# Kernel tuning notes

Hardware: AMD Instinct MI355X
Metric: run time of the kernel (lower is better)

The kernel has to match this reference:

```python
import jax, jax.numpy as jnp
import numpy as np

EPS_KERNEL = 1e-4   # eps added inside softmax_kernel exp
EPS_DENOM = 1e-6    # eps added to k_cumsum in the denominator
N_CHUNKS = 128      # matches torch.chunk(128, dim=-2) in causal_linear_attention_noncuda


def gaussian_orthogonal_random_matrix(nb_rows, nb_cols, rng):
    # scaling=0: rows are orthogonal blocks scaled by chi-distributed norms
    n_full = nb_rows // nb_cols + (1 if nb_rows % nb_cols else 0)
    blocks = []
    for _ in range(n_full):
        g = rng.standard_normal((nb_cols, nb_cols))
        qmat, _ = np.linalg.qr(g)
        blocks.append(qmat.T)
    mat = np.concatenate(blocks, axis=0)[:nb_rows]
    multiplier = np.linalg.norm(rng.standard_normal((nb_rows, nb_cols)), axis=1)
    return (multiplier[:, None] * mat).astype(np.float32)


def softmax_kernel(x, proj, is_query):
    # x: [b,h,n,d], proj: [m,d] -> phi(x): [b,h,n,m]
    d = x.shape[-1]
    normalizer = d ** -0.25
    ratio = proj.shape[0] ** -0.5
    xd = jnp.einsum('bhnd,md->bhnm', normalizer * x, proj)
    diag = 0.5 * (normalizer ** 2) * jnp.sum(x * x, axis=-1, keepdims=True)  # [b,h,n,1]
    if is_query:
        mx = jnp.max(xd, axis=-1, keepdims=True)
    else:
        mx = jnp.max(xd, axis=(-1, -2), keepdims=True)
    return ratio * (jnp.exp(xd - diag - mx) + EPS_KERNEL)


def causal_linear_attention(q, k, v):
    # q,k: [b,h,n,m] phi-features; v: [b,h,n,d]
    b, h, n, m = q.shape
    d = v.shape[-1]
    c = n // N_CHUNKS  # chunk length

    def chunked(t):
        return jnp.moveaxis(t.reshape(b, h, N_CHUNKS, c, t.shape[-1]), 2, 0)

    qc, kc, vc = chunked(q), chunked(k), chunked(v)  # [nc,b,h,c,*]

    def step(carry, inp):
        k_last, ctx_last = carry  # [b,h,m], [b,h,m,d]
        qi, ki, vi = inp
        k_cum = k_last[:, :, None, :] + jnp.cumsum(ki, axis=2)            # [b,h,c,m]
        d_inv = 1.0 / jnp.einsum('bhcm,bhcm->bhc', qi, k_cum + EPS_DENOM)
        ctx = jnp.einsum('bhcm,bhcd->bhcmd', ki, vi)                      # [b,h,c,m,d]
        ctx_cum = ctx_last[:, :, None, :, :] + jnp.cumsum(ctx, axis=2)
        out = jnp.einsum('bhcmd,bhcm,bhc->bhcd', ctx_cum, qi, d_inv)
        return (k_cum[:, :, -1], ctx_cum[:, :, -1]), out

    init = (jnp.zeros((b, h, m), q.dtype), jnp.zeros((b, h, m, d), q.dtype))
    _, outs = jax.lax.scan(jax.checkpoint(step), init, (qc, kc, vc))
    return jnp.moveaxis(outs, 0, 2).reshape(b, h, n, d)


def setup_inputs() -> dict:
    key = jax.random.key(0)
    kq, kk, kv = jax.random.split(key, 3)
    shape = (2, 8, 2048, 64)  # [batch, heads, seq, dim_heads]
    q = jax.random.normal(kq, shape, dtype=jnp.float32)
    k = jax.random.normal(kk, shape, dtype=jnp.float32)
    v = jax.random.normal(kv, shape, dtype=jnp.float32)
    proj = jnp.asarray(gaussian_orthogonal_random_matrix(256, 64, np.random.default_rng(0)))
    return {"q": q, "k": k, "v": v, "projection_matrix": proj}


def reference(q, k, v, projection_matrix):
    q_prime = softmax_kernel(q, projection_matrix, is_query=True)
    k_prime = softmax_kernel(k, projection_matrix, is_query=False)
    return causal_linear_attention(q_prime, k_prime, v)
```

## Files before the change

kernel.cpp:

```cpp
#include <hip/hip_runtime.h>
#include <hip/hip_bf16.h>
#include <cstddef>

typedef __attribute__((ext_vector_type(8))) short bf16x8;
typedef __attribute__((ext_vector_type(4))) float f32x4;

#define NCH_ 512
#define NRM_ 0.35355339059327373f
#define RATIO_ 0.0625f
#define EPSC_ 6.25e-6f
#define MFMA(a,b,c) __builtin_amdgcn_mfma_f32_16x16x32_bf16((a),(b),(c),0,0,0)

__device__ __forceinline__ unsigned short f2b(float f) {
  unsigned u = __float_as_uint(f);
  u += 0x7FFFu + ((u >> 16) & 1u);
  return (unsigned short)(u >> 16);
}
__device__ __forceinline__ float b2f(unsigned short h) {
  return __uint_as_float(((unsigned)h) << 16);
}
__device__ __forceinline__ unsigned pk2f(float a, float b) {
  union { __hip_bfloat162 h; unsigned u; } cv;
  cv.h = __float22bfloat162_rn(make_float2(a, b));
  return cv.u;
}
__device__ __forceinline__ float sumsq4(float4 a){ return a.x*a.x+a.y*a.y+a.z*a.z+a.w*a.w; }

__device__ __forceinline__ void arrive(unsigned* cnt) {
  __syncthreads();
  if (threadIdx.x == 0) {
    __threadfence();
    __hip_atomic_fetch_add(cnt, 1u, __ATOMIC_RELEASE, __HIP_MEMORY_SCOPE_AGENT);
  }
}
__device__ __forceinline__ void wait_for(unsigned* cnt, unsigned goal) {
  if (threadIdx.x == 0) {
    while (__hip_atomic_load(cnt, __ATOMIC_RELAXED, __HIP_MEMORY_SCOPE_AGENT) < goal)
      __builtin_amdgcn_s_sleep(4);
    __threadfence();
  }
  __syncthreads();
}

__global__ __launch_bounds__(256, 2) void fused_kernel(
    const float* __restrict__ qg, const float* __restrict__ kg,
    const float* __restrict__ vg, const float* __restrict__ projg,
    unsigned short* __restrict__ kvxP, unsigned short* __restrict__ sxP,
    float* __restrict__ blockmax, float* __restrict__ vsumG,
    float* __restrict__ out_g, unsigned* __restrict__ cnts)
{
  __shared__ unsigned short R0[256*72];
  __shared__ unsigned short XB[128*72];
  __shared__ unsigned short C_[80*72];
  __shared__ float diagK[64];
  __shared__ float diagQ[64];
  __shared__ float rmS[4*64];
  __shared__ float cmS[4];
  __shared__ float schS;
  const int t=threadIdx.x, ch=blockIdx.x;
  const int row0 = ch*64;
  const int lane=t&63, m16=lane&15, q4=lane>>4, w=t>>6;
  const int f0 = w*64, r0 = w*16;
  const int bh_own = ch>>5;
  unsigned* cntA = cnts;
  unsigned* cntS = cnts + 16;
  unsigned short* KX = XB;
  unsigned short* QX = XB + 64*72;
  unsigned short* kpT = XB;

#pragma unroll
  for (int i=0;i<8;++i){ int flat=i*2048+t*8; int f=flat>>6, d2=flat&63;
    float4 p0 = *(const float4*)(projg+flat);
    float4 p1 = *(const float4*)(projg+flat+4);
    *(uint4*)&R0[f*72+d2] = make_uint4(pk2f(p0.x,p0.y),pk2f(p0.z,p0.w),
                                       pk2f(p1.x,p1.y),pk2f(p1.z,p1.w)); }
  {
    const float* xg = kg + (size_t)row0*64;
#pragma unroll
    for (int i=0;i<4;++i){
      int flat=i*1024+t*4; int r=flat>>6, d2=flat&63;
      float4 f = *(const float4*)(xg+flat);
      float ss = sumsq4(f);
      ss += __shfl_xor(ss,1); ss += __shfl_xor(ss,2);
      ss += __shfl_xor(ss,4); ss += __shfl_xor(ss,8);
      if ((t&15)==0) diagK[r] = 0.0625f*ss;
      *(uint2*)&KX[r*72+d2] = make_uint2(pk2f(NRM_*f.x,NRM_*f.y), pk2f(NRM_*f.z,NRM_*f.w));
    }
  }
  {
    const float* xg = qg + (size_t)row0*64;
#pragma unroll
    for (int i=0;i<4;++i){
      int flat=i*1024+t*4; int r=flat>>6, d2=flat&63;
      float4 f = *(const float4*)(xg+flat);
      float ss = sumsq4(f);
      ss += __shfl_xor(ss,1); ss += __shfl_xor(ss,2);
      ss += __shfl_xor(ss,4); ss += __shfl_xor(ss,8);
      if ((t&15)==0) diagQ[r] = 0.0625f*ss;
      *(uint2*)&QX[r*72+d2] = make_uint2(pk2f(NRM_*f.x,NRM_*f.y), pk2f(NRM_*f.z,NRM_*f.w));
    }
  }
  {
    int c = t&63, sq_ = t>>6;
#pragma unroll
    for (int i=0;i<16;++i)
      C_[c*72 + sq_*16 + i] = f2b(vg[((size_t)row0 + sq_*16 + i)*64 + c]);
    int cc = 64 + (t>>4), s4 = (t&15)*4;
    unsigned short hv = (cc==64) ? (unsigned short)0x3F80 : (unsigned short)0;
    unsigned pv = (unsigned)hv | ((unsigned)hv<<16);
    *(uint2*)&C_[cc*72 + s4] = make_uint2(pv, pv);
  }
  __syncthreads();

  if (t < 80) {
    float s = 0.f;
#pragma unroll 16
    for (int i=0;i<64;++i) s += b2f(C_[t*72+i]);
    vsumG[(size_t)ch*80 + t] = s;
  }

  bf16x8 bk[4][2], bq[4][2]; float dk4[4], dq4[4];
#pragma unroll
  for (int rt=0;rt<4;++rt){
    bk[rt][0] = *(const bf16x8*)&KX[(rt*16+m16)*72 + q4*8];
    bk[rt][1] = *(const bf16x8*)&KX[(rt*16+m16)*72 + 32 + q4*8];
    bq[rt][0] = *(const bf16x8*)&QX[(rt*16+m16)*72 + q4*8];
    bq[rt][1] = *(const bf16x8*)&QX[(rt*16+m16)*72 + 32 + q4*8];
    dk4[rt] = diagK[rt*16+m16];
    dq4[rt] = diagQ[rt*16+m16];
  }
  f32x4 kacc[4][4], qacc[4][4];
#pragma unroll
  for (int rt=0;rt<4;++rt)
#pragma unroll
    for (int mt=0;mt<4;++mt){ kacc[rt][mt] = (f32x4){0.f,0.f,0.f,0.f};
                              qacc[rt][mt] = (f32x4){0.f,0.f,0.f,0.f}; }
#pragma unroll
  for (int kk=0;kk<2;++kk)
#pragma unroll
    for (int mt=0;mt<4;++mt){
      bf16x8 a = *(const bf16x8*)&R0[(f0+mt*16+m16)*72 + kk*32 + q4*8];
#pragma unroll
      for (int rt=0;rt<4;++rt){
        kacc[rt][mt] = MFMA(a, bk[rt][kk], kacc[rt][mt]);
        qacc[rt][mt] = MFMA(a, bq[rt][kk], qacc[rt][mt]);
      }
    }
  {
    float mx = kacc[0][0][0];
#pragma unroll
    for (int rt=0;rt<4;++rt)
#pragma unroll
      for (int mt=0;mt<4;++mt)
#pragma unroll
        for (int j=0;j<4;++j) mx = fmaxf(mx, kacc[rt][mt][j]);
#pragma unroll
    for (int off=1; off<64; off<<=1) mx = fmaxf(mx, __shfl_xor(mx, off));
    if (lane == 0) cmS[w] = mx;
  }
#pragma unroll
  for (int rt=0;rt<4;++rt){
    float p = qacc[rt][0][0];
#pragma unroll
    for (int mt=0;mt<4;++mt)
#pragma unroll
      for (int j=0;j<4;++j) p = fmaxf(p, qacc[rt][mt][j]);
    p = fmaxf(p, __shfl_xor(p,16)); p = fmaxf(p, __shfl_xor(p,32));
    if (q4 == 0) rmS[w*64 + rt*16+m16] = p;
  }
  __syncthreads();
  const float cmax = fmaxf(fmaxf(cmS[0],cmS[1]),fmaxf(cmS[2],cmS[3]));
  if (t == 0) blockmax[ch] = cmax;

  unsigned short* qS = R0;
#pragma unroll
  for (int rt=0;rt<4;++rt){
    int rr = rt*16+m16;
    float rm = fmaxf(fmaxf(rmS[rr],rmS[64+rr]),fmaxf(rmS[128+rr],rmS[192+rr]));
    float e = dq4[rt] + rm;
#pragma unroll
    for (int mt=0;mt<4;++mt){
      float v0 = RATIO_*(__expf(qacc[rt][mt][0]-e)+1e-4f);
      float v1 = RATIO_*(__expf(qacc[rt][mt][1]-e)+1e-4f);
      float v2 = RATIO_*(__expf(qacc[rt][mt][2]-e)+1e-4f);
      float v3 = RATIO_*(__expf(qacc[rt][mt][3]-e)+1e-4f);
      *(uint2*)&qS[rr*264 + f0 + mt*16 + q4*4] = make_uint2(pk2f(v0,v1), pk2f(v2,v3));
    }
  }
  __syncthreads();
  bf16x8 aq[8];
#pragma unroll
  for (int kk=0;kk<8;++kk)
    aq[kk] = *(const bf16x8*)&qS[(r0+m16)*264 + kk*32 + q4*8];
  float q1v = 0.f;
#pragma unroll
  for (int kk=0;kk<8;++kk){
    union { bf16x8 v; unsigned u[4]; } av; av.v = aq[kk];
#pragma unroll
    for (int i=0;i<4;++i)
      q1v += b2f((unsigned short)av.u[i]) + b2f((unsigned short)(av.u[i]>>16));
  }
  q1v += __shfl_xor(q1v,16); q1v += __shfl_xor(q1v,32);
  __syncthreads();

  unsigned short* kpS = R0;
  unsigned kpx[4][4][2];
#pragma unroll
  for (int rt=0;rt<4;++rt){
    float e = dk4[rt] + cmax;
    int rr = rt*16+m16;
#pragma unroll
    for (int mt=0;mt<4;++mt){
      float v0 = RATIO_*__expf(kacc[rt][mt][0]-e);
      float v1 = RATIO_*__expf(kacc[rt][mt][1]-e);
      float v2 = RATIO_*__expf(kacc[rt][mt][2]-e);
      float v3 = RATIO_*__expf(kacc[rt][mt][3]-e);
      kpx[rt][mt][0] = pk2f(v0,v1); kpx[rt][mt][1] = pk2f(v2,v3);
      *(uint2*)&kpS[rr*264 + f0 + mt*16 + q4*4] = make_uint2(kpx[rt][mt][0], kpx[rt][mt][1]);
    }
  }
  if ((w>>1) == 0) {
#pragma unroll
    for (int rt=0;rt<4;++rt)
#pragma unroll
      for (int mt=0;mt<4;++mt)
#pragma unroll
        for (int jp=0;jp<2;++jp){
          int frl = (w&1)*64 + mt*16 + q4*4 + jp*2;
          unsigned uv = kpx[rt][mt][jp];
          kpT[frl*72 + rt*16+m16]     = (unsigned short)uv;
          kpT[(frl+1)*72 + rt*16+m16] = (unsigned short)(uv>>16);
        }
  }
  __syncthreads();
#pragma unroll
  for (int h=0; h<2; ++h) {
    if (h == 1) {
      __syncthreads();
      if ((w>>1) == 1) {
#pragma unroll
        for (int rt=0;rt<4;++rt)
#pragma unroll
          for (int mt=0;mt<4;++mt)
#pragma unroll
            for (int jp=0;jp<2;++jp){
              int frl = (w&1)*64 + mt*16 + q4*4 + jp*2;
              unsigned uv = kpx[rt][mt][jp];
              kpT[frl*72 + rt*16+m16]     = (unsigned short)uv;
              kpT[(frl+1)*72 + rt*16+m16] = (unsigned short)(uv>>16);
            }
      }
      __syncthreads();
    }
    f32x4 c2a[5][2];
#pragma unroll
    for (int ct=0;ct<5;++ct)
#pragma unroll
      for (int p=0;p<2;++p) c2a[ct][p] = (f32x4){0.f,0.f,0.f,0.f};
#pragma unroll
    for (int kk=0;kk<2;++kk){
      bf16x8 av[5];
#pragma unroll
      for (int ct=0;ct<5;++ct)
        av[ct] = *(const bf16x8*)&C_[(ct*16+m16)*72 + kk*32 + q4*8];
#pragma unroll
      for (int p=0;p<2;++p){
        int mtl = w*2 + p;
        bf16x8 bv = *(const bf16x8*)&kpT[(mtl*16+m16)*72 + kk*32 + q4*8];
#pragma unroll
        for (int ct=0;ct<5;++ct)
          c2a[ct][p] = MFMA(av[ct], bv, c2a[ct][p]);
      }
    }
#pragma unroll
    for (int ct=0;ct<5;++ct)
#pragma unroll
      for (int p=0;p<2;++p){
        int mtg = h*8 + w*2 + p;
        int mrow = mtg*16 + m16;
        int fb = (mrow>>5)*512 + ((mrow>>3)&3)*8 + (mrow&7);
        unsigned short* dst = kvxP + (size_t)(ch*5+ct)*4096 + fb + (q4*4)*32;
#pragma unroll
        for (int j=0;j<4;++j)
          dst[j*32] = f2b(c2a[ct][p][j]);
      }
    if (h == 0) __syncthreads();
  }

  arrive(&cntA[bh_own]);

  if (ch < 320) {
    const int qtr = ch & 3, ct5 = (ch>>2)%5, bhs = ch/20;
    wait_for(&cntA[bhs], 32u);
    float* sS  = (float*)XB;
    float* vsS = ((float*)XB) + 32;
    if (t < 32) {
      float bm = blockmax[bhs*32 + t];
      float km = bm;
#pragma unroll
      for (int off=16; off>=1; off>>=1) km = fmaxf(km, __shfl_xor(km, off));
      sS[t] = __expf(bm - km);
    }
    for (int i=t; i<512; i+=256){
      int chl = i>>4, c16 = i&15;
      vsS[chl*16+c16] = vsumG[(size_t)(bhs*32+chl)*80 + ct5*16 + c16];
    }
    __syncthreads();
    const int fbase = qtr*1024 + t*4;
    const int c16t = (t>>3)&15;
    const bool isEps = (ct5==4) && (c16t == 1);
    float carry0=0.f, carry1=0.f, carry2=0.f, carry3=0.f;
    const size_t stride = (size_t)5*4096;
    size_t base = ((size_t)(bhs*32)*5 + ct5)*4096 + fbase;
#pragma unroll 8
    for (int chl=0; chl<32; ++chl){
      unsigned s0, s1;
      if (isEps) { unsigned ee = pk2f(1e-6f,1e-6f); s0 = ee; s1 = ee; }
      else { s0 = pk2f(carry0,carry1); s1 = pk2f(carry2,carry3); }
      *(uint2*)(sxP + base) = make_uint2(s0, s1);
      uint2 raw = *(const uint2*)(kvxP + base);
      float sc_ = sS[chl];
      float evs = EPSC_ * vsS[chl*16+c16t];
      carry0 += sc_*b2f((unsigned short)(raw.x))     + evs;
      carry1 += sc_*b2f((unsigned short)(raw.x>>16)) + evs;
      carry2 += sc_*b2f((unsigned short)(raw.y))     + evs;
      carry3 += sc_*b2f((unsigned short)(raw.y>>16)) + evs;
      base += stride;
    }
    arrive(&cntS[bhs]);
  }

  wait_for(&cntS[bh_own], 20u);

  if (t < 32) {
    float bm = blockmax[bh_own*32 + t];
    float km = bm;
#pragma unroll
    for (int off=16; off>=1; off>>=1) km = fmaxf(km, __shfl_xor(km, off));
    if (t == (ch & 31)) schS = __expf(bm - km);
  }

  f32x4 accA[4], accO[5];
#pragma unroll
  for (int i=0;i<4;++i) accA[i] = (f32x4){0.f,0.f,0.f,0.f};
#pragma unroll
  for (int i=0;i<5;++i) accO[i] = (f32x4){0.f,0.f,0.f,0.f};
  const unsigned short* sxb = sxP + (size_t)ch*5*4096 + m16*32 + q4*8;
#pragma unroll
  for (int kk=0;kk<8;++kk){
    bf16x8 a = aq[kk];
#pragma unroll
    for (int st=0;st<4;++st){
      bf16x8 bfr = *(const bf16x8*)&kpS[(st*16+m16)*264 + kk*32 + q4*8];
      accA[st] = MFMA(a, bfr, accA[st]);
    }
#pragma unroll
    for (int ct=0;ct<5;++ct)
      accO[ct] = MFMA(a, *(const bf16x8*)(sxb + (size_t)ct*4096 + kk*512), accO[ct]);
  }
  __syncthreads();
  const float sch = schS;
  unsigned short* P = XB;
#pragma unroll
  for (int j=0;j<4;++j){
    int rr = r0 + q4*4 + j;
    float q1r = __shfl(q1v, q4*4 + j);
    float addc = EPSC_ * q1r;
#pragma unroll
    for (int st=0;st<4;++st){
      int cc = st*16 + m16;
      P[rr*72 + cc] = f2b((cc<=rr) ? (sch*accA[st][j] + addc) : 0.f);
    }
  }
#pragma unroll
  for (int k2=0;k2<2;++k2){
    bf16x8 aP = *(const bf16x8*)&P[(r0+m16)*72 + k2*32 + q4*8];
#pragma unroll
    for (int ct=0;ct<5;++ct){
      bf16x8 bfr = *(const bf16x8*)&C_[(ct*16+m16)*72 + k2*32 + q4*8];
      accO[ct] = MFMA(aP, bfr, accO[ct]);
    }
  }
  __syncthreads();
  float* oT = (float*)R0;
#pragma unroll
  for (int j=0;j<4;++j){
    float d64 = __shfl(accO[4][j], (lane & 48));
    float d65 = __shfl(accO[4][j], (lane & 48) | 1);
    float dinv = 1.f/(d64+d65);
    int rr = r0 + q4*4 + j;
#pragma unroll
    for (int ct=0;ct<4;++ct)
      oT[rr*68 + ct*16 + m16] = accO[ct][j]*dinv;
  }
  __syncthreads();
#pragma unroll
  for (int i=0;i<4;++i){ int flat=i*1024+t*4; int r=flat>>6, c2=flat&63;
    *(float4*)(out_g + (size_t)row0*64 + flat) = *(const float4*)&oT[r*68+c2]; }
}


__global__ __launch_bounds__(256, 2) void kfeat_kernel(
    const float* __restrict__ kg, const float* __restrict__ vg,
    const float* __restrict__ projg,
    unsigned short* __restrict__ kvxP,
    float* __restrict__ blockmax, float* __restrict__ vsumG)
{
  __shared__ unsigned short R0[256*72];
  __shared__ unsigned short XB[128*72];
  __shared__ unsigned short C_[80*72];
  __shared__ float diagS[64];
  __shared__ float rmS[4];
  const int t=threadIdx.x, ch=blockIdx.x;
  const int row0 = ch*64;
  const int lane=t&63, m16=lane&15, q4=lane>>4, w=t>>6;
  const int f0 = w*64;
  unsigned short* kpS = R0;
  unsigned short* xbS = XB;
  unsigned short* kpT = XB;

#pragma unroll
  for (int i=0;i<8;++i){ int flat=i*2048+t*8; int f=flat>>6, d2=flat&63;
    float4 p0 = *(const float4*)(projg+flat);
    float4 p1 = *(const float4*)(projg+flat+4);
    *(uint4*)&R0[f*72+d2] = make_uint4(pk2f(p0.x,p0.y),pk2f(p0.z,p0.w),
                                       pk2f(p1.x,p1.y),pk2f(p1.z,p1.w)); }
  {
    const float* xg = kg + (size_t)row0*64;
#pragma unroll
    for (int i=0;i<4;++i){
      int flat=i*1024+t*4; int r=flat>>6, d2=flat&63;
      float4 f = *(const float4*)(xg+flat);
      float ss = sumsq4(f);
      ss += __shfl_xor(ss,1); ss += __shfl_xor(ss,2);
      ss += __shfl_xor(ss,4); ss += __shfl_xor(ss,8);
      if ((t&15)==0) diagS[r] = 0.0625f*ss;
      *(uint2*)&xbS[r*72+d2] = make_uint2(pk2f(NRM_*f.x,NRM_*f.y), pk2f(NRM_*f.z,NRM_*f.w));
    }
  }
  {
    int c = t&63, sq_ = t>>6;
#pragma unroll
    for (int i=0;i<16;++i)
      C_[c*72 + sq_*16 + i] = f2b(vg[((size_t)row0 + sq_*16 + i)*64 + c]);
    int cc = 64 + (t>>4), s4 = (t&15)*4;
    unsigned short hv = (cc==64) ? (unsigned short)0x3F80 : (unsigned short)0;
    unsigned pv = (unsigned)hv | ((unsigned)hv<<16);
    *(uint2*)&C_[cc*72 + s4] = make_uint2(pv, pv);
  }
  __syncthreads();

  if (t < 80) {
    float s = 0.f;
#pragma unroll 16
    for (int i=0;i<64;++i) s += b2f(C_[t*72+i]);
    vsumG[(size_t)ch*80 + t] = s;
  }

  bf16x8 b[4][2]; float diag4[4];
#pragma unroll
  for (int rt=0;rt<4;++rt){
    b[rt][0] = *(const bf16x8*)&xbS[(rt*16+m16)*72 + q4*8];
    b[rt][1] = *(const bf16x8*)&xbS[(rt*16+m16)*72 + 32 + q4*8];
    diag4[rt] = diagS[rt*16+m16];
  }
  f32x4 acc[4][4];
#pragma unroll
  for (int rt=0;rt<4;++rt)
#pragma unroll
    for (int mt=0;mt<4;++mt) acc[rt][mt] = (f32x4){0.f,0.f,0.f,0.f};
#pragma unroll
  for (int kk=0;kk<2;++kk)
#pragma unroll
    for (int mt=0;mt<4;++mt){
      bf16x8 a = *(const bf16x8*)&R0[(f0+mt*16+m16)*72 + kk*32 + q4*8];
#pragma unroll
      for (int rt=0;rt<4;++rt)
        acc[rt][mt] = MFMA(a, b[rt][kk], acc[rt][mt]);
    }
  {
    float mx = acc[0][0][0];
#pragma unroll
    for (int rt=0;rt<4;++rt)
#pragma unroll
      for (int mt=0;mt<4;++mt)
#pragma unroll
        for (int j=0;j<4;++j) mx = fmaxf(mx, acc[rt][mt][j]);
#pragma unroll
    for (int off=1; off<64; off<<=1) mx = fmaxf(mx, __shfl_xor(mx, off));
    if (lane == 0) rmS[w] = mx;
  }
  __syncthreads();
  const float cmax = fmaxf(fmaxf(rmS[0],rmS[1]),fmaxf(rmS[2],rmS[3]));
  if (t == 0) blockmax[ch] = cmax;

  unsigned kpx[4][4][2];
#pragma unroll
  for (int rt=0;rt<4;++rt){
    float e = diag4[rt] + cmax;
    int rr = rt*16+m16;
#pragma unroll
    for (int mt=0;mt<4;++mt){
      float v0 = RATIO_*__expf(acc[rt][mt][0]-e);
      float v1 = RATIO_*__expf(acc[rt][mt][1]-e);
      float v2 = RATIO_*__expf(acc[rt][mt][2]-e);
      float v3 = RATIO_*__expf(acc[rt][mt][3]-e);
      kpx[rt][mt][0] = pk2f(v0,v1); kpx[rt][mt][1] = pk2f(v2,v3);
      *(uint2*)&kpS[rr*264 + f0 + mt*16 + q4*4] = make_uint2(kpx[rt][mt][0], kpx[rt][mt][1]);
    }
  }
  if ((w>>1) == 0) {
#pragma unroll
    for (int rt=0;rt<4;++rt)
#pragma unroll
      for (int mt=0;mt<4;++mt)
#pragma unroll
        for (int jp=0;jp<2;++jp){
          int frl = (w&1)*64 + mt*16 + q4*4 + jp*2;
          unsigned uv = kpx[rt][mt][jp];
          kpT[frl*72 + rt*16+m16]     = (unsigned short)uv;
          kpT[(frl+1)*72 + rt*16+m16] = (unsigned short)(uv>>16);
        }
  }
  __syncthreads();
#pragma unroll
  for (int h=0; h<2; ++h) {
    if (h == 1) {
      __syncthreads();
      if ((w>>1) == 1) {
#pragma unroll
        for (int rt=0;rt<4;++rt)
#pragma unroll
          for (int mt=0;mt<4;++mt)
#pragma unroll
            for (int jp=0;jp<2;++jp){
              int frl = (w&1)*64 + mt*16 + q4*4 + jp*2;
              unsigned uv = kpx[rt][mt][jp];
              kpT[frl*72 + rt*16+m16]     = (unsigned short)uv;
              kpT[(frl+1)*72 + rt*16+m16] = (unsigned short)(uv>>16);
            }
      }
      __syncthreads();
    }
    f32x4 c2a[5][2];
#pragma unroll
    for (int ct=0;ct<5;++ct)
#pragma unroll
      for (int p=0;p<2;++p) c2a[ct][p] = (f32x4){0.f,0.f,0.f,0.f};
#pragma unroll
    for (int kk=0;kk<2;++kk){
      bf16x8 av[5];
#pragma unroll
      for (int ct=0;ct<5;++ct)
        av[ct] = *(const bf16x8*)&C_[(ct*16+m16)*72 + kk*32 + q4*8];
#pragma unroll
      for (int p=0;p<2;++p){
        int mtl = w*2 + p;
        bf16x8 bv = *(const bf16x8*)&kpT[(mtl*16+m16)*72 + kk*32 + q4*8];
#pragma unroll
        for (int ct=0;ct<5;++ct)
          c2a[ct][p] = MFMA(av[ct], bv, c2a[ct][p]);
      }
    }
#pragma unroll
    for (int ct=0;ct<5;++ct)
#pragma unroll
      for (int p=0;p<2;++p){
        int mtg = h*8 + w*2 + p;
        int mrow = mtg*16 + m16;
        int fb = (mrow>>5)*512 + ((mrow>>3)&3)*8 + (mrow&7);
        unsigned short* dst = kvxP + (size_t)(ch*5+ct)*4096 + fb + (q4*4)*32;
#pragma unroll
        for (int j=0;j<4;++j)
          dst[j*32] = f2b(c2a[ct][p][j]);
      }
    if (h == 0) __syncthreads();
  }
}

__global__ __launch_bounds__(256, 4) void scan_kernel(
    const unsigned short* __restrict__ kvxP, unsigned short* __restrict__ sxP,
    const float* __restrict__ blockmax, const float* __restrict__ vsumG)
{
  __shared__ float sS[32];
  __shared__ float vsS[32][16];
  const int t = threadIdx.x, bid = blockIdx.x;
  const int qtr = bid & 3, ct = (bid>>2)%5, bh = bid/20;
  if (t < 32) {
    float bm = blockmax[bh*32 + t];
    float km = bm;
#pragma unroll
    for (int off=16; off>=1; off>>=1) km = fmaxf(km, __shfl_xor(km, off));
    sS[t] = __expf(bm - km);
  }
  for (int i=t; i<512; i+=256){
    int chl = i>>4, c16 = i&15;
    vsS[chl][c16] = vsumG[(size_t)(bh*32+chl)*80 + ct*16 + c16];
  }
  __syncthreads();
  const int fbase = qtr*1024 + t*4;
  const int c16t = (t>>3)&15;
  const bool isEps = (ct==4) && (c16t == 1);
  float carry0=0.f, carry1=0.f, carry2=0.f, carry3=0.f;
  const size_t stride = (size_t)5*4096;
  size_t base = ((size_t)(bh*32)*5 + ct)*4096 + fbase;
#pragma unroll 4
  for (int chl=0; chl<32; ++chl){
    unsigned s0, s1;
    if (isEps) { unsigned ee = pk2f(1e-6f,1e-6f); s0 = ee; s1 = ee; }
    else { s0 = pk2f(carry0,carry1); s1 = pk2f(carry2,carry3); }
    *(uint2*)(sxP + base) = make_uint2(s0, s1);
    uint2 raw = *(const uint2*)(kvxP + base);
    float sch = sS[chl];
    float evs = EPSC_ * vsS[chl][c16t];
    carry0 += sch*b2f((unsigned short)(raw.x))     + evs;
    carry1 += sch*b2f((unsigned short)(raw.x>>16)) + evs;
    carry2 += sch*b2f((unsigned short)(raw.y))     + evs;
    carry3 += sch*b2f((unsigned short)(raw.y>>16)) + evs;
    base += stride;
  }
}

__global__ __launch_bounds__(256, 2) void out_kernel(
    const float* __restrict__ qg, const float* __restrict__ kg,
    const float* __restrict__ projg, const unsigned short* __restrict__ sxP,
    const float* __restrict__ vg, const float* __restrict__ blockmax,
    float* __restrict__ out_g)
{
  __shared__ unsigned short R0[256*72];
  __shared__ unsigned short KX[64*72];
  __shared__ unsigned short QX[64*72];
  __shared__ unsigned short C_[80*72];
  __shared__ float diagK[64];
  __shared__ float diagQ[64];
  __shared__ float rmS[4*64];
  __shared__ float cmS[4];
  __shared__ float schS;
  const int t=threadIdx.x, ch=blockIdx.x;
  const int row0 = ch*64;
  const int lane=t&63, m16=lane&15, q4=lane>>4, w=t>>6;
  const int f0 = w*64, r0 = w*16;
  unsigned short* P = KX;

#pragma unroll
  for (int i=0;i<8;++i){ int flat=i*2048+t*8; int f=flat>>6, d2=flat&63;
    float4 p0 = *(const float4*)(projg+flat);
    float4 p1 = *(const float4*)(projg+flat+4);
    *(uint4*)&R0[f*72+d2] = make_uint4(pk2f(p0.x,p0.y),pk2f(p0.z,p0.w),
                                       pk2f(p1.x,p1.y),pk2f(p1.z,p1.w)); }
  {
    const float* xg = kg + (size_t)row0*64;
#pragma unroll
    for (int i=0;i<4;++i){
      int flat=i*1024+t*4; int r=flat>>6, d2=flat&63;
      float4 f = *(const float4*)(xg+flat);
      float ss = sumsq4(f);
      ss += __shfl_xor(ss,1); ss += __shfl_xor(ss,2);
      ss += __shfl_xor(ss,4); ss += __shfl_xor(ss,8);
      if ((t&15)==0) diagK[r] = 0.0625f*ss;
      *(uint2*)&KX[r*72+d2] = make_uint2(pk2f(NRM_*f.x,NRM_*f.y), pk2f(NRM_*f.z,NRM_*f.w));
    }
  }
  {
    const float* xg = qg + (size_t)row0*64;
#pragma unroll
    for (int i=0;i<4;++i){
      int flat=i*1024+t*4; int r=flat>>6, d2=flat&63;
      float4 f = *(const float4*)(xg+flat);
      float ss = sumsq4(f);
      ss += __shfl_xor(ss,1); ss += __shfl_xor(ss,2);
      ss += __shfl_xor(ss,4); ss += __shfl_xor(ss,8);
      if ((t&15)==0) diagQ[r] = 0.0625f*ss;
      *(uint2*)&QX[r*72+d2] = make_uint2(pk2f(NRM_*f.x,NRM_*f.y), pk2f(NRM_*f.z,NRM_*f.w));
    }
  }
  {
    int c = t&63, sq_ = t>>6;
#pragma unroll
    for (int i=0;i<16;++i)
      C_[c*72 + sq_*16 + i] = f2b(vg[((size_t)row0 + sq_*16 + i)*64 + c]);
    int cc = 64 + (t>>4), s4 = (t&15)*4;
    unsigned short hv = (cc==64) ? (unsigned short)0x3F80 : (unsigned short)0;
    unsigned pv = (unsigned)hv | ((unsigned)hv<<16);
    *(uint2*)&C_[cc*72 + s4] = make_uint2(pv, pv);
  }
  if (t < 32) {
    float bm = blockmax[(ch>>5)*32 + t];
    float km = bm;
#pragma unroll
    for (int off=16; off>=1; off>>=1) km = fmaxf(km, __shfl_xor(km, off));
    if (t == (ch & 31)) schS = __expf(bm - km);
  }
  __syncthreads();

  bf16x8 bk[4][2], bq[4][2]; float dk4[4], dq4[4];
#pragma unroll
  for (int rt=0;rt<4;++rt){
    bk[rt][0] = *(const bf16x8*)&KX[(rt*16+m16)*72 + q4*8];
    bk[rt][1] = *(const bf16x8*)&KX[(rt*16+m16)*72 + 32 + q4*8];
    bq[rt][0] = *(const bf16x8*)&QX[(rt*16+m16)*72 + q4*8];
    bq[rt][1] = *(const bf16x8*)&QX[(rt*16+m16)*72 + 32 + q4*8];
    dk4[rt] = diagK[rt*16+m16];
    dq4[rt] = diagQ[rt*16+m16];
  }
  f32x4 kacc[4][4], qacc[4][4];
#pragma unroll
  for (int rt=0;rt<4;++rt)
#pragma unroll
    for (int mt=0;mt<4;++mt){ kacc[rt][mt] = (f32x4){0.f,0.f,0.f,0.f};
                              qacc[rt][mt] = (f32x4){0.f,0.f,0.f,0.f}; }
#pragma unroll
  for (int kk=0;kk<2;++kk)
#pragma unroll
    for (int mt=0;mt<4;++mt){
      bf16x8 a = *(const bf16x8*)&R0[(f0+mt*16+m16)*72 + kk*32 + q4*8];
#pragma unroll
      for (int rt=0;rt<4;++rt){
        kacc[rt][mt] = MFMA(a, bk[rt][kk], kacc[rt][mt]);
        qacc[rt][mt] = MFMA(a, bq[rt][kk], qacc[rt][mt]);
      }
    }
  {
    float mx = kacc[0][0][0];
#pragma unroll
    for (int rt=0;rt<4;++rt)
#pragma unroll
      for (int mt=0;mt<4;++mt)
#pragma unroll
        for (int j=0;j<4;++j) mx = fmaxf(mx, kacc[rt][mt][j]);
#pragma unroll
    for (int off=1; off<64; off<<=1) mx = fmaxf(mx, __shfl_xor(mx, off));
    if (lane == 0) cmS[w] = mx;
  }
#pragma unroll
  for (int rt=0;rt<4;++rt){
    float p = qacc[rt][0][0];
#pragma unroll
    for (int mt=0;mt<4;++mt)
#pragma unroll
      for (int j=0;j<4;++j) p = fmaxf(p, qacc[rt][mt][j]);
    p = fmaxf(p, __shfl_xor(p,16)); p = fmaxf(p, __shfl_xor(p,32));
    if (q4 == 0) rmS[w*64 + rt*16+m16] = p;
  }
  __syncthreads();
  const float cmax = fmaxf(fmaxf(cmS[0],cmS[1]),fmaxf(cmS[2],cmS[3]));

  unsigned short* qS = R0;
#pragma unroll
  for (int rt=0;rt<4;++rt){
    int rr = rt*16+m16;
    float rm = fmaxf(fmaxf(rmS[rr],rmS[64+rr]),fmaxf(rmS[128+rr],rmS[192+rr]));
    float e = dq4[rt] + rm;
#pragma unroll
    for (int mt=0;mt<4;++mt){
      float v0 = RATIO_*(__expf(qacc[rt][mt][0]-e)+1e-4f);
      float v1 = RATIO_*(__expf(qacc[rt][mt][1]-e)+1e-4f);
      float v2 = RATIO_*(__expf(qacc[rt][mt][2]-e)+1e-4f);
      float v3 = RATIO_*(__expf(qacc[rt][mt][3]-e)+1e-4f);
      *(uint2*)&qS[rr*264 + f0 + mt*16 + q4*4] = make_uint2(pk2f(v0,v1), pk2f(v2,v3));
    }
  }
  __syncthreads();
  bf16x8 aq[8];
#pragma unroll
  for (int kk=0;kk<8;++kk)
    aq[kk] = *(const bf16x8*)&qS[(r0+m16)*264 + kk*32 + q4*8];
  float q1v = 0.f;
#pragma unroll
  for (int kk=0;kk<8;++kk){
    union { bf16x8 v; unsigned u[4]; } av; av.v = aq[kk];
#pragma unroll
    for (int i=0;i<4;++i)
      q1v += b2f((unsigned short)av.u[i]) + b2f((unsigned short)(av.u[i]>>16));
  }
  q1v += __shfl_xor(q1v,16); q1v += __shfl_xor(q1v,32);
  __syncthreads();

  unsigned short* kpS = R0;
#pragma unroll
  for (int rt=0;rt<4;++rt){
    float e = dk4[rt] + cmax;
    int rr = rt*16+m16;
#pragma unroll
    for (int mt=0;mt<4;++mt){
      float v0 = RATIO_*__expf(kacc[rt][mt][0]-e);
      float v1 = RATIO_*__expf(kacc[rt][mt][1]-e);
      float v2 = RATIO_*__expf(kacc[rt][mt][2]-e);
      float v3 = RATIO_*__expf(kacc[rt][mt][3]-e);
      *(uint2*)&kpS[rr*264 + f0 + mt*16 + q4*4] = make_uint2(pk2f(v0,v1), pk2f(v2,v3));
    }
  }
  __syncthreads();

  f32x4 accA[4], accO[5];
#pragma unroll
  for (int i=0;i<4;++i) accA[i] = (f32x4){0.f,0.f,0.f,0.f};
#pragma unroll
  for (int i=0;i<5;++i) accO[i] = (f32x4){0.f,0.f,0.f,0.f};
  const unsigned short* sxb = sxP + (size_t)ch*5*4096 + m16*32 + q4*8;
#pragma unroll
  for (int kk=0;kk<8;++kk){
    bf16x8 a = aq[kk];
#pragma unroll
    for (int st=0;st<4;++st){
      bf16x8 bfr = *(const bf16x8*)&kpS[(st*16+m16)*264 + kk*32 + q4*8];
      accA[st] = MFMA(a, bfr, accA[st]);
    }
#pragma unroll
    for (int ct=0;ct<5;++ct)
      accO[ct] = MFMA(a, *(const bf16x8*)(sxb + (size_t)ct*4096 + kk*512), accO[ct]);
  }
  __syncthreads();
  const float sch = schS;
#pragma unroll
  for (int j=0;j<4;++j){
    int rr = r0 + q4*4 + j;
    float q1r = __shfl(q1v, q4*4 + j);
    float addc = EPSC_ * q1r;
#pragma unroll
    for (int st=0;st<4;++st){
      int cc = st*16 + m16;
      P[rr*72 + cc] = f2b((cc<=rr) ? (sch*accA[st][j] + addc) : 0.f);
    }
  }
#pragma unroll
  for (int k2=0;k2<2;++k2){
    bf16x8 aP = *(const bf16x8*)&P[(r0+m16)*72 + k2*32 + q4*8];
#pragma unroll
    for (int ct=0;ct<5;++ct){
      bf16x8 bfr = *(const bf16x8*)&C_[(ct*16+m16)*72 + k2*32 + q4*8];
      accO[ct] = MFMA(aP, bfr, accO[ct]);
    }
  }
  __syncthreads();
  float* oT = (float*)R0;
#pragma unroll
  for (int j=0;j<4;++j){
    float d64 = __shfl(accO[4][j], (lane & 48));
    float d65 = __shfl(accO[4][j], (lane & 48) | 1);
    float dinv = 1.f/(d64+d65);
    int rr = r0 + q4*4 + j;
#pragma unroll
    for (int ct=0;ct<4;++ct)
      oT[rr*68 + ct*16 + m16] = accO[ct][j]*dinv;
  }
  __syncthreads();
#pragma unroll
  for (int i=0;i<4;++i){ int flat=i*1024+t*4; int r=flat>>6, c2=flat&63;
    *(float4*)(out_g + (size_t)row0*64 + flat) = *(const float4*)&oT[r*68+c2]; }
}

extern "C" void kernel_launch(void* const* d_in, const int* in_sizes, int n_in,
                              void* d_out, int out_size, void* d_ws, size_t ws_size,
                              hipStream_t stream)
{
  (void)in_sizes; (void)n_in; (void)out_size; (void)ws_size;
  const float* q    = (const float*)d_in[0];
  const float* k    = (const float*)d_in[1];
  const float* v    = (const float*)d_in[2];
  const float* proj = (const float*)d_in[3];
  float* out = (float*)d_out;

  char* p8 = (char*)d_ws;
  unsigned short* kvxP = (unsigned short*)p8; p8 += (size_t)NCH_*5*4096*2;
  unsigned short* sxP  = (unsigned short*)p8; p8 += (size_t)NCH_*5*4096*2;
  float* blockmax = (float*)p8; p8 += NCH_*sizeof(float);
  float* vsumG    = (float*)p8; p8 += (size_t)NCH_*80*sizeof(float);
  unsigned* cnts  = (unsigned*)p8;

  static int fused_ok = -1;
  if (fused_ok < 0) {
    int nb = 0;
    hipError_t e = hipOccupancyMaxActiveBlocksPerMultiprocessor(&nb, fused_kernel,
                                                                256, (size_t)0);
    fused_ok = (e == hipSuccess && nb >= 2) ? 1 : 0;
  }

  if (fused_ok) {
    hipMemsetAsync(cnts, 0, 32*sizeof(unsigned), stream);
    fused_kernel<<<dim3(NCH_), dim3(256), 0, stream>>>(q, k, v, proj, kvxP, sxP,
                                                       blockmax, vsumG, out, cnts);
  } else {
    kfeat_kernel<<<dim3(NCH_), dim3(256), 0, stream>>>(k, v, proj, kvxP,
                                                       blockmax, vsumG);
    scan_kernel <<<dim3(320),  dim3(256), 0, stream>>>(kvxP, sxP, blockmax, vsumG);
    out_kernel  <<<dim3(NCH_), dim3(256), 0, stream>>>(q, k, proj, sxP, v,
                                                       blockmax, out);
  }
}
```

Baseline: 115.2 us.

## Double fused kernel block to 512 threads and split phases across wave groups

Raises the fused kernel from 256 to 512 threads (8 waves), halving per-wave feature-projection work. The intra-chunk attention MFMAs go to one wave group and the inter-chunk state MFMAs to the other. This aims to add latency hiding and cut per-wave register pressure so the cooperative kernel runs faster. The cost is an extra barrier and idle waves in the serial scan and output phases, and the grid-wide spin-wait scheme now depends on enough 512-thread blocks being co-resident.

```diff
diff --git a/kernel.cpp b/kernel.cpp
--- a/kernel.cpp
+++ b/kernel.cpp
@@ -42,7 +42,7 @@
   __syncthreads();
 }
 
-__global__ __launch_bounds__(256, 2) void fused_kernel(
+__global__ __launch_bounds__(512, 4) void fused_kernel(
     const float* __restrict__ qg, const float* __restrict__ kg,
     const float* __restrict__ vg, const float* __restrict__ projg,
     unsigned short* __restrict__ kvxP, unsigned short* __restrict__ sxP,
@@ -54,13 +54,15 @@
   __shared__ unsigned short C_[80*72];
   __shared__ float diagK[64];
   __shared__ float diagQ[64];
-  __shared__ float rmS[4*64];
-  __shared__ float cmS[4];
+  __shared__ float rmS[8*64];
+  __shared__ float cmS[8];
   __shared__ float schS;
   const int t=threadIdx.x, ch=blockIdx.x;
   const int row0 = ch*64;
   const int lane=t&63, m16=lane&15, q4=lane>>4, w=t>>6;
-  const int f0 = w*64, r0 = w*16;
+  const int f0 = w*32;
+  const int rw = (w&3)*16;
+  const int g  = w>>2;
   const int bh_own = ch>>5;
   unsigned* cntA = cnts;
   unsigned* cntS = cnts + 16;
@@ -69,7 +71,7 @@
   unsigned short* kpT = XB;
 
 #pragma unroll
-  for (int i=0;i<8;++i){ int flat=i*2048+t*8; int f=flat>>6, d2=flat&63;
+  for (int i=0;i<4;++i){ int flat=i*4096+t*8; int f=flat>>6, d2=flat&63;
     float4 p0 = *(const float4*)(projg+flat);
     float4 p1 = *(const float4*)(projg+flat+4);
     *(uint4*)&R0[f*72+d2] = make_uint4(pk2f(p0.x,p0.y),pk2f(p0.z,p0.w),
@@ -77,8 +79,8 @@
   {
     const float* xg = kg + (size_t)row0*64;
 #pragma unroll
-    for (int i=0;i<4;++i){
-      int flat=i*1024+t*4; int r=flat>>6, d2=flat&63;
+    for (int i=0;i<2;++i){
+      int flat=i*2048+t*4; int r=flat>>6, d2=flat&63;
       float4 f = *(const float4*)(xg+flat);
       float ss = sumsq4(f);
       ss += __shfl_xor(ss,1); ss += __shfl_xor(ss,2);
@@ -90,8 +92,8 @@
   {
     const float* xg = qg + (size_t)row0*64;
 #pragma unroll
-    for (int i=0;i<4;++i){
-      int flat=i*1024+t*4; int r=flat>>6, d2=flat&63;
+    for (int i=0;i<2;++i){
+      int flat=i*2048+t*4; int r=flat>>6, d2=flat&63;
       float4 f = *(const float4*)(xg+flat);
       float ss = sumsq4(f);
       ss += __shfl_xor(ss,1); ss += __shfl_xor(ss,2);
@@ -103,12 +105,14 @@
   {
     int c = t&63, sq_ = t>>6;
 #pragma unroll
-    for (int i=0;i<16;++i)
-      C_[c*72 + sq_*16 + i] = f2b(vg[((size_t)row0 + sq_*16 + i)*64 + c]);
-    int cc = 64 + (t>>4), s4 = (t&15)*4;
-    unsigned short hv = (cc==64) ? (unsigned short)0x3F80 : (unsigned short)0;
-    unsigned pv = (unsigned)hv | ((unsigned)hv<<16);
-    *(uint2*)&C_[cc*72 + s4] = make_uint2(pv, pv);
+    for (int i=0;i<8;++i)
+      C_[c*72 + sq_*8 + i] = f2b(vg[((size_t)row0 + sq_*8 + i)*64 + c]);
+    if (t < 256) {
+      int cc = 64 + (t>>4), s4 = (t&15)*4;
+      unsigned short hv = (cc==64) ? (unsigned short)0x3F80 : (unsigned short)0;
+      unsigned pv = (unsigned)hv | ((unsigned)hv<<16);
+      *(uint2*)&C_[cc*72 + s4] = make_uint2(pv, pv);
+    }
   }
   __syncthreads();
 
@@ -119,39 +123,55 @@
     vsumG[(size_t)ch*80 + t] = s;
   }
 
-  bf16x8 bk[4][2], bq[4][2]; float dk4[4], dq4[4];
-#pragma unroll
-  for (int rt=0;rt<4;++rt){
-    bk[rt][0] = *(const bf16x8*)&KX[(rt*16+m16)*72 + q4*8];
-    bk[rt][1] = *(const bf16x8*)&KX[(rt*16+m16)*72 + 32 + q4*8];
-    bq[rt][0] = *(const bf16x8*)&QX[(rt*16+m16)*72 + q4*8];
-    bq[rt][1] = *(const bf16x8*)&QX[(rt*16+m16)*72 + 32 + q4*8];
-    dk4[rt] = diagK[rt*16+m16];
-    dq4[rt] = diagQ[rt*16+m16];
-  }
-  f32x4 kacc[4][4], qacc[4][4];
+  float dk4[4], dq4[4];
+#pragma unroll
+  for (int rt=0;rt<4;++rt){ dk4[rt] = diagK[rt*16+m16]; dq4[rt] = diagQ[rt*16+m16]; }
+  f32x4 kacc[4][2], qacc[4][2];
 #pragma unroll
   for (int rt=0;rt<4;++rt)
 #pragma unroll
-    for (int mt=0;mt<4;++mt){ kacc[rt][mt] = (f32x4){0.f,0.f,0.f,0.f};
+    for (int mt=0;mt<2;++mt){ kacc[rt][mt] = (f32x4){0.f,0.f,0.f,0.f};
                               qacc[rt][mt] = (f32x4){0.f,0.f,0.f,0.f}; }
-#pragma unroll
-  for (int kk=0;kk<2;++kk)
-#pragma unroll
-    for (int mt=0;mt<4;++mt){
-      bf16x8 a = *(const bf16x8*)&R0[(f0+mt*16+m16)*72 + kk*32 + q4*8];
-#pragma unroll
-      for (int rt=0;rt<4;++rt){
-        kacc[rt][mt] = MFMA(a, bk[rt][kk], kacc[rt][mt]);
-        qacc[rt][mt] = MFMA(a, bq[rt][kk], qacc[rt][mt]);
-      }
-    }
+  {
+    bf16x8 bk[4][2];
+#pragma unroll
+    for (int rt=0;rt<4;++rt){
+      bk[rt][0] = *(const bf16x8*)&KX[(rt*16+m16)*72 + q4*8];
+      bk[rt][1] = *(const bf16x8*)&KX[(rt*16+m16)*72 + 32 + q4*8];
+    }
+#pragma unroll
+    for (int kk=0;kk<2;++kk)
+#pragma unroll
+      for (int mt=0;mt<2;++mt){
+        bf16x8 a = *(const bf16x8*)&R0[(f0+mt*16+m16)*72 + kk*32 + q4*8];
+#pragma unroll
+        for (int rt=0;rt<4;++rt)
+          kacc[rt][mt] = MFMA(a, bk[rt][kk], kacc[rt][mt]);
+      }
+  }
+  {
+    bf16x8 bq[4][2];
+#pragma unroll
+    for (int rt=0;rt<4;++rt){
+      bq[rt][0] = *(const bf16x8*)&QX[(rt*16+m16)*72 + q4*8];
+      bq[rt][1] = *(const bf16x8*)&QX[(rt*16+m16)*72 + 32 + q4*8];
+    }
+#pragma unroll
+    for (int kk=0;kk<2;++kk)
+#pragma unroll
+      for (int mt=0;mt<2;++mt){
+        bf16x8 a = *(const bf16x8*)&R0[(f0+mt*16+m16)*72 + kk*32 + q4*8];
+#pragma unroll
+        for (int rt=0;rt<4;++rt)
+          qacc[rt][mt] = MFMA(a, bq[rt][kk], qacc[rt][mt]);
+      }
+  }
   {
     float mx = kacc[0][0][0];
 #pragma unroll
     for (int rt=0;rt<4;++rt)
 #pragma unroll
-      for (int mt=0;mt<4;++mt)
+      for (int mt=0;mt<2;++mt)
 #pragma unroll
         for (int j=0;j<4;++j) mx = fmaxf(mx, kacc[rt][mt][j]);
 #pragma unroll
@@ -162,24 +182,28 @@
   for (int rt=0;rt<4;++rt){
     float p = qacc[rt][0][0];
 #pragma unroll
-    for (int mt=0;mt<4;++mt)
+    for (int mt=0;mt<2;++mt)
 #pragma unroll
       for (int j=0;j<4;++j) p = fmaxf(p, qacc[rt][mt][j]);
     p = fmaxf(p, __shfl_xor(p,16)); p = fmaxf(p, __shfl_xor(p,32));
     if (q4 == 0) rmS[w*64 + rt*16+m16] = p;
   }
   __syncthreads();
-  const float cmax = fmaxf(fmaxf(cmS[0],cmS[1]),fmaxf(cmS[2],cmS[3]));
+  float cmax = cmS[0];
+#pragma unroll
+  for (int s=1;s<8;++s) cmax = fmaxf(cmax, cmS[s]);
   if (t == 0) blockmax[ch] = cmax;
 
   unsigned short* qS = R0;
 #pragma unroll
   for (int rt=0;rt<4;++rt){
     int rr = rt*16+m16;
-    float rm = fmaxf(fmaxf(rmS[rr],rmS[64+rr]),fmaxf(rmS[128+rr],rmS[192+rr]));
+    float rm = rmS[rr];
+#pragma unroll
+    for (int s=1;s<8;++s) rm = fmaxf(rm, rmS[s*64+rr]);
     float e = dq4[rt] + rm;
 #pragma unroll
-    for (int mt=0;mt<4;++mt){
+    for (int mt=0;mt<2;++mt){
       float v0 = RATIO_*(__expf(qacc[rt][mt][0]-e)+1e-4f);
       float v1 = RATIO_*(__expf(qacc[rt][mt][1]-e)+1e-4f);
       float v2 = RATIO_*(__expf(qacc[rt][mt][2]-e)+1e-4f);
@@ -191,7 +215,7 @@
   bf16x8 aq[8];
 #pragma unroll
   for (int kk=0;kk<8;++kk)
-    aq[kk] = *(const bf16x8*)&qS[(r0+m16)*264 + kk*32 + q4*8];
+    aq[kk] = *(const bf16x8*)&qS[(rw+m16)*264 + kk*32 + q4*8];
   float q1v = 0.f;
 #pragma unroll
   for (int kk=0;kk<8;++kk){
@@ -204,13 +228,13 @@
   __syncthreads();
 
   unsigned short* kpS = R0;
-  unsigned kpx[4][4][2];
+  unsigned kpx[4][2][2];
 #pragma unroll
   for (int rt=0;rt<4;++rt){
     float e = dk4[rt] + cmax;
     int rr = rt*16+m16;
 #pragma unroll
-    for (int mt=0;mt<4;++mt){
+    for (int mt=0;mt<2;++mt){
       float v0 = RATIO_*__expf(kacc[rt][mt][0]-e);
       float v1 = RATIO_*__expf(kacc[rt][mt][1]-e);
       float v2 = RATIO_*__expf(kacc[rt][mt][2]-e);
@@ -219,14 +243,14 @@
       *(uint2*)&kpS[rr*264 + f0 + mt*16 + q4*4] = make_uint2(kpx[rt][mt][0], kpx[rt][mt][1]);
     }
   }
-  if ((w>>1) == 0) {
+  if (g == 0) {
 #pragma unroll
     for (int rt=0;rt<4;++rt)
 #pragma unroll
-      for (int mt=0;mt<4;++mt)
+      for (int mt=0;mt<2;++mt)
 #pragma unroll
         for (int jp=0;jp<2;++jp){
-          int frl = (w&1)*64 + mt*16 + q4*4 + jp*2;
+          int frl = (w&3)*32 + mt*16 + q4*4 + jp*2;
           unsigned uv = kpx[rt][mt][jp];
           kpT[frl*72 + rt*16+m16]     = (unsigned short)uv;
           kpT[(frl+1)*72 + rt*16+m16] = (unsigned short)(uv>>16);
@@ -237,14 +261,14 @@
   for (int h=0; h<2; ++h) {
     if (h == 1) {
       __syncthreads();
-      if ((w>>1) == 1) {
+      if (g == 1) {
 #pragma unroll
         for (int rt=0;rt<4;++rt)
 #pragma unroll
-          for (int mt=0;mt<4;++mt)
+          for (int mt=0;mt<2;++mt)
 #pragma unroll
             for (int jp=0;jp<2;++jp){
-              int frl = (w&1)*64 + mt*16 + q4*4 + jp*2;
+              int frl = (w&3)*32 + mt*16 + q4*4 + jp*2;
               unsigned uv = kpx[rt][mt][jp];
               kpT[frl*72 + rt*16+m16]     = (unsigned short)uv;
               kpT[(frl+1)*72 + rt*16+m16] = (unsigned short)(uv>>16);
@@ -252,38 +276,28 @@
       }
       __syncthreads();
     }
-    f32x4 c2a[5][2];
-#pragma unroll
-    for (int ct=0;ct<5;++ct)
-#pragma unroll
-      for (int p=0;p<2;++p) c2a[ct][p] = (f32x4){0.f,0.f,0.f,0.f};
+    f32x4 c2a[5];
+#pragma unroll
+    for (int ct=0;ct<5;++ct) c2a[ct] = (f32x4){0.f,0.f,0.f,0.f};
 #pragma unroll
     for (int kk=0;kk<2;++kk){
-      bf16x8 av[5];
-#pragma unroll
-      for (int ct=0;ct<5;++ct)
-        av[ct] = *(const bf16x8*)&C_[(ct*16+m16)*72 + kk*32 + q4*8];
-#pragma unroll
-      for (int p=0;p<2;++p){
-        int mtl = w*2 + p;
-        bf16x8 bv = *(const bf16x8*)&kpT[(mtl*16+m16)*72 + kk*32 + q4*8];
-#pragma unroll
-        for (int ct=0;ct<5;++ct)
-          c2a[ct][p] = MFMA(av[ct], bv, c2a[ct][p]);
-      }
-    }
-#pragma unroll
-    for (int ct=0;ct<5;++ct)
-#pragma unroll
-      for (int p=0;p<2;++p){
-        int mtg = h*8 + w*2 + p;
-        int mrow = mtg*16 + m16;
-        int fb = (mrow>>5)*512 + ((mrow>>3)&3)*8 + (mrow&7);
-        unsigned short* dst = kvxP + (size_t)(ch*5+ct)*4096 + fb + (q4*4)*32;
-#pragma unroll
-        for (int j=0;j<4;++j)
-          dst[j*32] = f2b(c2a[ct][p][j]);
-      }
+      bf16x8 bv = *(const bf16x8*)&kpT[(w*16+m16)*72 + kk*32 + q4*8];
+#pragma unroll
+      for (int ct=0;ct<5;++ct){
+        bf16x8 av = *(const bf16x8*)&C_[(ct*16+m16)*72 + kk*32 + q4*8];
+        c2a[ct] = MFMA(av, bv, c2a[ct]);
+      }
+    }
+#pragma unroll
+    for (int ct=0;ct<5;++ct){
+      int mtg = h*8 + w;
+      int mrow = mtg*16 + m16;
+      int fb = (mrow>>5)*512 + ((mrow>>3)&3)*8 + (mrow&7);
+      unsigned short* dst = kvxP + (size_t)(ch*5+ct)*4096 + fb + (q4*4)*32;
+#pragma unroll
+      for (int j=0;j<4;++j)
+        dst[j*32] = f2b(c2a[ct][j]);
+    }
     if (h == 0) __syncthreads();
   }
 
@@ -301,31 +315,33 @@
       for (int off=16; off>=1; off>>=1) km = fmaxf(km, __shfl_xor(km, off));
       sS[t] = __expf(bm - km);
     }
-    for (int i=t; i<512; i+=256){
-      int chl = i>>4, c16 = i&15;
+    {
+      int chl = t>>4, c16 = t&15;
       vsS[chl*16+c16] = vsumG[(size_t)(bhs*32+chl)*80 + ct5*16 + c16];
     }
     __syncthreads();
-    const int fbase = qtr*1024 + t*4;
-    const int c16t = (t>>3)&15;
-    const bool isEps = (ct5==4) && (c16t == 1);
-    float carry0=0.f, carry1=0.f, carry2=0.f, carry3=0.f;
-    const size_t stride = (size_t)5*4096;
-    size_t base = ((size_t)(bhs*32)*5 + ct5)*4096 + fbase;
+    if (t < 256) {
+      const int fbase = qtr*1024 + t*4;
+      const int c16t = (t>>3)&15;
+      const bool isEps = (ct5==4) && (c16t == 1);
+      float carry0=0.f, carry1=0.f, carry2=0.f, carry3=0.f;
+      const size_t stride = (size_t)5*4096;
+      size_t base = ((size_t)(bhs*32)*5 + ct5)*4096 + fbase;
 #pragma unroll 8
-    for (int chl=0; chl<32; ++chl){
-      unsigned s0, s1;
-      if (isEps) { unsigned ee = pk2f(1e-6f,1e-6f); s0 = ee; s1 = ee; }
-      else { s0 = pk2f(carry0,carry1); s1 = pk2f(carry2,carry3); }
-      *(uint2*)(sxP + base) = make_uint2(s0, s1);
-      uint2 raw = *(const uint2*)(kvxP + base);
-      float sc_ = sS[chl];
-      float evs = EPSC_ * vsS[chl*16+c16t];
-      carry0 += sc_*b2f((unsigned short)(raw.x))     + evs;
-      carry1 += sc_*b2f((unsigned short)(raw.x>>16)) + evs;
-      carry2 += sc_*b2f((unsigned short)(raw.y))     + evs;
-      carry3 += sc_*b2f((unsigned short)(raw.y>>16)) + evs;
-      base += stride;
+      for (int chl=0; chl<32; ++chl){
+        unsigned s0, s1;
+        if (isEps) { unsigned ee = pk2f(1e-6f,1e-6f); s0 = ee; s1 = ee; }
+        else { s0 = pk2f(carry0,carry1); s1 = pk2f(carry2,carry3); }
+        *(uint2*)(sxP + base) = make_uint2(s0, s1);
+        uint2 raw = *(const uint2*)(kvxP + base);
+        float sc_ = sS[chl];
+        float evs = EPSC_ * vsS[chl*16+c16t];
+        carry0 += sc_*b2f((unsigned short)(raw.x))     + evs;
+        carry1 += sc_*b2f((unsigned short)(raw.x>>16)) + evs;
+        carry2 += sc_*b2f((unsigned short)(raw.y))     + evs;
+        carry3 += sc_*b2f((unsigned short)(raw.y>>16)) + evs;
+        base += stride;
+      }
     }
     arrive(&cntS[bhs]);
   }
@@ -345,58 +361,72 @@
   for (int i=0;i<4;++i) accA[i] = (f32x4){0.f,0.f,0.f,0.f};
 #pragma unroll
   for (int i=0;i<5;++i) accO[i] = (f32x4){0.f,0.f,0.f,0.f};
-  const unsigned short* sxb = sxP + (size_t)ch*5*4096 + m16*32 + q4*8;
-#pragma unroll
-  for (int kk=0;kk<8;++kk){
-    bf16x8 a = aq[kk];
-#pragma unroll
-    for (int st=0;st<4;++st){
-      bf16x8 bfr = *(const bf16x8*)&kpS[(st*16+m16)*264 + kk*32 + q4*8];
-      accA[st] = MFMA(a, bfr, accA[st]);
-    }
-#pragma unroll
-    for (int ct=0;ct<5;++ct)
-      accO[ct] = MFMA(a, *(const bf16x8*)(sxb + (size_t)ct*4096 + kk*512), accO[ct]);
+  if (g == 0) {
+#pragma unroll
+    for (int kk=0;kk<8;++kk){
+      bf16x8 a = aq[kk];
+#pragma unroll
+      for (int st=0;st<4;++st){
+        bf16x8 bfr = *(const bf16x8*)&kpS[(st*16+m16)*264 + kk*32 + q4*8];
+        accA[st] = MFMA(a, bfr, accA[st]);
+      }
+    }
+  } else {
+    const unsigned short* sxb = sxP + (size_t)ch*5*4096 + m16*32 + q4*8;
+#pragma unroll
+    for (int kk=0;kk<8;++kk){
+      bf16x8 a = aq[kk];
+#pragma unroll
+      for (int ct=0;ct<5;++ct)
+        accO[ct] = MFMA(a, *(const bf16x8*)(sxb + (size_t)ct*4096 + kk*512), accO[ct]);
+    }
   }
   __syncthreads();
   const float sch = schS;
   unsigned short* P = XB;
-#pragma unroll
-  for (int j=0;j<4;++j){
-    int rr = r0 + q4*4 + j;
-    float q1r = __shfl(q1v, q4*4 + j);
-    float addc = EPSC_ * q1r;
-#pragma unroll
-    for (int st=0;st<4;++st){
-      int cc = st*16 + m16;
-      P[rr*72 + cc] = f2b((cc<=rr) ? (sch*accA[st][j] + addc) : 0.f);
-    }
-  }
-#pragma unroll
-  for (int k2=0;k2<2;++k2){
-    bf16x8 aP = *(const bf16x8*)&P[(r0+m16)*72 + k2*32 + q4*8];
-#pragma unroll
-    for (int ct=0;ct<5;++ct){
-      bf16x8 bfr = *(const bf16x8*)&C_[(ct*16+m16)*72 + k2*32 + q4*8];
-      accO[ct] = MFMA(aP, bfr, accO[ct]);
-    }
-  }
-  __syncthreads();
-  float* oT = (float*)R0;
-#pragma unroll
-  for (int j=0;j<4;++j){
-    float d64 = __shfl(accO[4][j], (lane & 48));
-    float d65 = __shfl(accO[4][j], (lane & 48) | 1);
-    float dinv = 1.f/(d64+d65);
-    int rr = r0 + q4*4 + j;
-#pragma unroll
-    for (int ct=0;ct<4;++ct)
-      oT[rr*68 + ct*16 + m16] = accO[ct][j]*dinv;
-  }
-  __syncthreads();
-#pragma unroll
-  for (int i=0;i<4;++i){ int flat=i*1024+t*4; int r=flat>>6, c2=flat&63;
-    *(float4*)(out_g + (size_t)row0*64 + flat) = *(const float4*)&oT[r*68+c2]; }
+  if (g == 0) {
+#pragma unroll
+    for (int j=0;j<4;++j){
+      int rr = rw + q4*4 + j;
+      float q1r = __shfl(q1v, q4*4 + j);
+      float addc = EPSC_ * q1r;
+#pragma unroll
+      for (int st=0;st<4;++st){
+        int cc = st*16 + m16;
+        P[rr*72 + cc] = f2b((cc<=rr) ? (sch*accA[st][j] + addc) : 0.f);
+      }
+    }
+  }
+  __syncthreads();
+  if (g == 1) {
+#pragma unroll
+    for (int k2=0;k2<2;++k2){
+      bf16x8 aP = *(const bf16x8*)&P[(rw+m16)*72 + k2*32 + q4*8];
+#pragma unroll
+      for (int ct=0;ct<5;++ct){
+        bf16x8 bfr = *(const bf16x8*)&C_[(ct*16+m16)*72 + k2*32 + q4*8];
+        accO[ct] = MFMA(aP, bfr, accO[ct]);
+      }
+    }
+    float* oT = (float*)R0;
+#pragma unroll
+    for (int j=0;j<4;++j){
+      float d64 = __shfl(accO[4][j], (lane & 48));
+      float d65 = __shfl(accO[4][j], (lane & 48) | 1);
+      float dinv = 1.f/(d64+d65);
+      int rr = rw + q4*4 + j;
+#pragma unroll
+      for (int ct=0;ct<4;++ct)
+        oT[rr*68 + ct*16 + m16] = accO[ct][j]*dinv;
+    }
+  }
+  __syncthreads();
+  {
+    const float* oT = (const float*)R0;
+#pragma unroll
+    for (int i=0;i<2;++i){ int flat=i*2048+t*4; int r=flat>>6, c2=flat&63;
+      *(float4*)(out_g + (size_t)row0*64 + flat) = *(const float4*)&oT[r*68+c2]; }
+  }
 }
 
 
@@ -872,13 +902,13 @@
   if (fused_ok < 0) {
     int nb = 0;
     hipError_t e = hipOccupancyMaxActiveBlocksPerMultiprocessor(&nb, fused_kernel,
-                                                                256, (size_t)0);
+                                                                512, (size_t)0);
     fused_ok = (e == hipSuccess && nb >= 2) ? 1 : 0;
   }
 
   if (fused_ok) {
     hipMemsetAsync(cnts, 0, 32*sizeof(unsigned), stream);
-    fused_kernel<<<dim3(NCH_), dim3(256), 0, stream>>>(q, k, v, proj, kvxP, sxP,
+    fused_kernel<<<dim3(NCH_), dim3(512), 0, stream>>>(q, k, v, proj, kvxP, sxP,
                                                        blockmax, vsumG, out, cnts);
   } else {
     kfeat_kernel<<<dim3(NCH_), dim3(256), 0, stream>>>(k, v, proj, kvxP,
```

Result: no change. 114.5 us (-0.6%).
